# Optimization experiments

Hardware: AMD Instinct MI355X
Metric: run time of the kernel (lower is better)

The kernel has to match this reference:

```python
import jax, jax.numpy as jnp
import numpy as np

D_MODEL = 2048
N_HEADS = 16
D_HEAD = D_MODEL // N_HEADS
D_FF = 4 * D_MODEL
LN_EPS = 1e-5


def setup_inputs() -> dict:
    key = jax.random.key(0)
    ks = jax.random.split(key, 12)
    s = 1.0 / np.sqrt(D_MODEL)
    sf = 1.0 / np.sqrt(D_FF)
    return {
        "x": jax.random.normal(ks[0], (1, 2048, D_MODEL), dtype=jnp.float32),
        "ln1_g": jnp.ones((D_MODEL,), jnp.float32),
        "ln1_b": jnp.zeros((D_MODEL,), jnp.float32),
        # weights stored [in, out] (transpose of torch layout; equivalent under random init)
        "Wq": jax.random.normal(ks[1], (D_MODEL, D_MODEL), jnp.float32) * s,
        "Wk": jax.random.normal(ks[2], (D_MODEL, D_MODEL), jnp.float32) * s,
        "Wv": jax.random.normal(ks[3], (D_MODEL, D_MODEL), jnp.float32) * s,
        "Wp": jax.random.normal(ks[4], (D_MODEL, D_MODEL), jnp.float32) * s,
        "bp": jnp.zeros((D_MODEL,), jnp.float32),
        "ln2_g": jnp.ones((D_MODEL,), jnp.float32),
        "ln2_b": jnp.zeros((D_MODEL,), jnp.float32),
        "W1": jax.random.normal(ks[5], (D_MODEL, D_FF), jnp.float32) * s,
        "b1": jnp.zeros((D_FF,), jnp.float32),
        "W2": jax.random.normal(ks[6], (D_FF, D_MODEL), jnp.float32) * sf,
        "b2": jnp.zeros((D_MODEL,), jnp.float32),
    }


def _layer_norm(x, g, b):
    mu = jnp.mean(x, axis=-1, keepdims=True)
    var = jnp.mean(jnp.square(x - mu), axis=-1, keepdims=True)
    return (x - mu) * jax.lax.rsqrt(var + LN_EPS) * g + b


def _attention(h, Wq, Wk, Wv, Wp, bp):
    B, S, E = h.shape
    q = (h @ Wq).reshape(B, S, N_HEADS, D_HEAD)
    k = (h @ Wk).reshape(B, S, N_HEADS, D_HEAD)
    v = (h @ Wv).reshape(B, S, N_HEADS, D_HEAD)
    # [B, H, S, S] causal scores (matches the naive materialized original)
    scores = jnp.einsum("bqhd,bkhd->bhqk", q, k) / np.sqrt(D_HEAD).astype(np.float32)
    causal = jnp.arange(S)[:, None] >= jnp.arange(S)[None, :]
    scores = jnp.where(causal, scores, -jnp.inf)
    attn = jax.nn.softmax(scores, axis=-1)
    out = jnp.einsum("bhqk,bkhd->bqhd", attn, v).reshape(B, S, E)
    return out @ Wp + bp


def reference(x, ln1_g, ln1_b, Wq, Wk, Wv, Wp, bp, ln2_g, ln2_b, W1, b1, W2, b2):
    # attention branch: x += MHA(LN1(x)); dropout=0 (inference)
    x1 = x + _attention(_layer_norm(x, ln1_g, ln1_b), Wq, Wk, Wv, Wp, bp)
    # ff branch: FeedForward adds its own residual on the normalized input
    g = _layer_norm(x1, ln2_g, ln2_b)
    mlp = jax.nn.gelu(g @ W1 + b1, approximate=False) @ W2 + b2
    return x1 + (g + mlp)
```

## Files before the change

kernel.cpp:

```cpp
#include <hip/hip_runtime.h>
#include <math.h>

typedef unsigned int u32;
typedef unsigned short u16;
typedef __attribute__((ext_vector_type(8))) short short8;
typedef __attribute__((ext_vector_type(4))) float f32x4;

__device__ __forceinline__ u16 f2bf(float f) {
  u32 u = __builtin_bit_cast(u32, f);
  u += 0x7FFFu + ((u >> 16) & 1u);
  return (u16)(u >> 16);
}
__device__ __forceinline__ float bf2f(u16 h) {
  u32 u = ((u32)h) << 16;
  return __builtin_bit_cast(float, u);
}
__device__ __forceinline__ void gload_lds16(const void* g, void* l) {
  __builtin_amdgcn_global_load_lds((const __attribute__((address_space(1))) u32*)g,
                                   (__attribute__((address_space(3))) u32*)l, 16, 0, 0);
}
__device__ __forceinline__ f32x4 mfma16(short8 a, short8 b, f32x4 c) {
  return __builtin_amdgcn_mfma_f32_16x16x32_bf16(a, b, c, 0, 0, 0);
}

__global__ __launch_bounds__(256) void transpose_cast(const float* __restrict__ src,
                                                      u16* __restrict__ dst, int K, int N) {
  __shared__ __attribute__((aligned(16))) u16 tile[64][72];
  const int n0 = blockIdx.x * 64, k0 = blockIdx.y * 64;
  const int t = threadIdx.x;
  const int tr = t >> 4;
  const int tc4 = (t & 15) * 4;
#pragma unroll
  for (int p = 0; p < 4; ++p) {
    int row = p * 16 + tr;
    const float4 v = *(const float4*)(src + (size_t)(k0 + row) * N + n0 + tc4);
    tile[tc4 + 0][row] = f2bf(v.x);
    tile[tc4 + 1][row] = f2bf(v.y);
    tile[tc4 + 2][row] = f2bf(v.z);
    tile[tc4 + 3][row] = f2bf(v.w);
  }
  __syncthreads();
  const int nr = t >> 2;
  const int kc = (t & 3) * 16;
  u16* d = dst + (size_t)(n0 + nr) * K + k0 + kc;
  *(short8*)(d) = *(const short8*)&tile[nr][kc];
  *(short8*)(d + 8) = *(const short8*)&tile[nr][kc + 8];
}

__global__ __launch_bounds__(256) void transpose_v(const u16* __restrict__ qkv,
                                                   u16* __restrict__ vT) {
  __shared__ __attribute__((aligned(16))) u16 tile[64][72];
  const int kv0 = blockIdx.x * 64, d0 = blockIdx.y * 64, h = blockIdx.z;
  const int t = threadIdx.x;
  const int tr = t >> 3;
  const int tc8 = (t & 7) * 8;
#pragma unroll
  for (int p = 0; p < 2; ++p) {
    int row = p * 32 + tr;
    short8 v = *(const short8*)(qkv + (size_t)(kv0 + row) * 6144 + 4096 + h * 128 + d0 + tc8);
#pragma unroll
    for (int j = 0; j < 8; ++j) tile[tc8 + j][row] = (u16)v[j];
  }
  __syncthreads();
  const int dr = t >> 2;
  const int kc = (t & 3) * 16;
  u16* dst = vT + ((size_t)h * 128 + d0 + dr) * 2048 + kv0 + kc;
  *(short8*)dst = *(const short8*)&tile[dr][kc];
  *(short8*)(dst + 8) = *(const short8*)&tile[dr][kc + 8];
}

__global__ __launch_bounds__(256) void ln_kernel(const float* __restrict__ x,
                                                 const float* __restrict__ gw,
                                                 const float* __restrict__ bw,
                                                 u16* __restrict__ out) {
  const int row = blockIdx.x, t = threadIdx.x;
  const float* xr = x + (size_t)row * 2048;
  const float4 v0 = *(const float4*)(xr + t * 8);
  const float4 v1 = *(const float4*)(xr + t * 8 + 4);
  float s = v0.x + v0.y + v0.z + v0.w + v1.x + v1.y + v1.z + v1.w;
  float q = v0.x * v0.x + v0.y * v0.y + v0.z * v0.z + v0.w * v0.w +
            v1.x * v1.x + v1.y * v1.y + v1.z * v1.z + v1.w * v1.w;
#pragma unroll
  for (int w = 32; w; w >>= 1) { s += __shfl_xor(s, w); q += __shfl_xor(q, w); }
  __shared__ float rs[4], rq[4];
  const int wid = t >> 6, lane = t & 63;
  if (!lane) { rs[wid] = s; rq[wid] = q; }
  __syncthreads();
  s = rs[0] + rs[1] + rs[2] + rs[3];
  q = rq[0] + rq[1] + rq[2] + rq[3];
  const float mu = s * (1.f / 2048.f);
  const float var = q * (1.f / 2048.f) - mu * mu;
  const float rstd = rsqrtf(var + 1e-5f);
  const float4 g0 = *(const float4*)(gw + t * 8);
  const float4 g1 = *(const float4*)(gw + t * 8 + 4);
  const float4 b0 = *(const float4*)(bw + t * 8);
  const float4 b1 = *(const float4*)(bw + t * 8 + 4);
  short8 o;
  o[0] = (short)f2bf((v0.x - mu) * rstd * g0.x + b0.x);
  o[1] = (short)f2bf((v0.y - mu) * rstd * g0.y + b0.y);
  o[2] = (short)f2bf((v0.z - mu) * rstd * g0.z + b0.z);
  o[3] = (short)f2bf((v0.w - mu) * rstd * g0.w + b0.w);
  o[4] = (short)f2bf((v1.x - mu) * rstd * g1.x + b1.x);
  o[5] = (short)f2bf((v1.y - mu) * rstd * g1.y + b1.y);
  o[6] = (short)f2bf((v1.z - mu) * rstd * g1.z + b1.z);
  o[7] = (short)f2bf((v1.w - mu) * rstd * g1.w + b1.w);
  *(short8*)(out + (size_t)row * 2048 + t * 8) = o;
}

template <int EPI>
__global__ __launch_bounds__(256) void gemm_kernel(const u16* __restrict__ A,
                                                   const u16* __restrict__ Bt,
                                                   int M, int N, int K, int Kc,
                                                   float* __restrict__ outF,
                                                   u16* __restrict__ outB,
                                                   const float* __restrict__ bias,
                                                   const float* __restrict__ res1,
                                                   const u16* __restrict__ res2,
                                                   float* __restrict__ pA,
                                                   float* __restrict__ pB) {
  __shared__ __attribute__((aligned(16))) u16 lsA[128 * 64];
  __shared__ __attribute__((aligned(16))) u16 lsB[128 * 64];
  const int m0 = blockIdx.y * 128, n0 = blockIdx.x * 128;
  const int tid = threadIdx.x, wid = tid >> 6, lane = tid & 63;
  const int wm = (wid >> 1) * 64, wn = (wid & 1) * 64;
  const int lq = lane & 15, lk = lane >> 4;
  const int rIn = lane >> 3, sIn = lane & 7;
  const int kStart = blockIdx.z * Kc;
  f32x4 acc[4][4] = {};

  for (int kt = kStart; kt < kStart + Kc; kt += 64) {
    if (kt != kStart) __syncthreads();
#pragma unroll
    for (int i = 0; i < 4; ++i) {
      int c = wid * 4 + i;
      int row = c * 8 + rIn;
      int scol = (sIn ^ (row & 7)) * 8;
      gload_lds16(A + (size_t)(m0 + row) * K + kt + scol, lsA + c * 512);
      gload_lds16(Bt + (size_t)(n0 + row) * K + kt + scol, lsB + c * 512);
    }
    __syncthreads();
#pragma unroll
    for (int kk = 0; kk < 2; ++kk) {
      short8 af[4], bfr[4];
#pragma unroll
      for (int i = 0; i < 4; ++i) {
        int ra = wm + i * 16 + lq;
        af[i] = *(const short8*)((const char*)lsA + ra * 128 +
                                 ((kk * 64 + lk * 16) ^ ((ra & 7) << 4)));
        int rb = wn + i * 16 + lq;
        bfr[i] = *(const short8*)((const char*)lsB + rb * 128 +
                                  ((kk * 64 + lk * 16) ^ ((rb & 7) << 4)));
      }
#pragma unroll
      for (int mi = 0; mi < 4; ++mi)
#pragma unroll
        for (int ni = 0; ni < 4; ++ni)
          acc[mi][ni] = mfma16(af[mi], bfr[ni], acc[mi][ni]);
    }
  }
  float* pp = nullptr;
  if (EPI == 4) {
    pp = (blockIdx.z < 2) ? pA : pB;
    pp += (size_t)(blockIdx.z & 1) * ((size_t)M * N);
  }
#pragma unroll
  for (int mi = 0; mi < 4; ++mi) {
#pragma unroll
    for (int ni = 0; ni < 4; ++ni) {
      const int col = n0 + wn + ni * 16 + lq;
#pragma unroll
      for (int r = 0; r < 4; ++r) {
        const int row = m0 + wm + mi * 16 + lk * 4 + r;
        const size_t idx = (size_t)row * N + col;
        float v = acc[mi][ni][r];
        if (EPI == 0) {
          outB[idx] = f2bf(v);
        } else if (EPI == 1) {
          outF[idx] = v + bias[col] + res1[idx];
        } else if (EPI == 2) {
          float xg = v + bias[col];
          outB[idx] = f2bf(0.5f * xg * (1.f + erff(xg * 0.70710678118654752f)));
        } else if (EPI == 3) {
          outF[idx] = v + bias[col] + res1[idx] + bf2f(res2[idx]);
        } else {
          pp[idx] = v;
        }
      }
    }
  }
}

template <int NS, int RES2>
__global__ __launch_bounds__(256) void reduce_kernel(const float* __restrict__ pA,
                                                     const float* __restrict__ pB,
                                                     const float* __restrict__ bias,
                                                     const float* __restrict__ res1,
                                                     const u16* __restrict__ res2,
                                                     float* __restrict__ out,
                                                     int MN, int N) {
  const int i = (blockIdx.x * 256 + threadIdx.x) * 4;
  if (i >= MN) return;
  float4 s = *(const float4*)(pA + i);
  {
    const float4 t = *(const float4*)(pA + MN + i);
    s.x += t.x; s.y += t.y; s.z += t.z; s.w += t.w;
  }
  if (NS == 4) {
    const float4 t0 = *(const float4*)(pB + i);
    const float4 t1 = *(const float4*)(pB + MN + i);
    s.x += t0.x + t1.x; s.y += t0.y + t1.y; s.z += t0.z + t1.z; s.w += t0.w + t1.w;
  }
  const int col = i & (N - 1);
  const float4 bv = *(const float4*)(bias + col);
  const float4 r1 = *(const float4*)(res1 + i);
  float4 o;
  o.x = s.x + bv.x + r1.x;
  o.y = s.y + bv.y + r1.y;
  o.z = s.z + bv.z + r1.z;
  o.w = s.w + bv.w + r1.w;
  if (RES2) {
    const u16* r2 = res2 + i;
    o.x += bf2f(r2[0]); o.y += bf2f(r2[1]); o.z += bf2f(r2[2]); o.w += bf2f(r2[3]);
  }
  *(float4*)(out + i) = o;
}

__global__ __launch_bounds__(256) void attn_kernel(const u16* __restrict__ qkv,
                                                   const u16* __restrict__ vT,
                                                   u16* __restrict__ attnout) {
  __shared__ __attribute__((aligned(16))) u16 lsK[64 * 128];
  __shared__ __attribute__((aligned(16))) u16 lsV[128 * 64];
  __shared__ __attribute__((aligned(16))) u16 lsP[4][16 * 64];
  const int h = blockIdx.y;
  const int qb = blockIdx.x * 64;
  const int tid = threadIdx.x, wid = tid >> 6, lane = tid & 63;
  const int lq = lane & 15, lk = lane >> 4;
  const int qw = qb + wid * 16;

  short8 qf[4];
  {
    const u16* qp = qkv + (size_t)(qw + lq) * 6144 + h * 128;
#pragma unroll
    for (int ks = 0; ks < 4; ++ks) qf[ks] = *(const short8*)(qp + ks * 32 + lk * 8);
  }
  float mreg[4], lreg[4];
  f32x4 o[8];
#pragma unroll
  for (int r = 0; r < 4; ++r) { mreg[r] = -INFINITY; lreg[r] = 0.f; }
#pragma unroll
  for (int dt = 0; dt < 8; ++dt) o[dt] = (f32x4){0.f, 0.f, 0.f, 0.f};

  const int rK = lane >> 4, sK = lane & 15;
  const int rV = lane >> 3, sV = lane & 7;
  const int nkt = qb / 64 + 1;
  for (int kt = 0; kt < nkt; ++kt) {
    const int kv0 = kt * 64;
    if (kt) __syncthreads();
#pragma unroll
    for (int i = 0; i < 4; ++i) {
      int c = wid * 4 + i;
      int rowK = c * 4 + rK;
      gload_lds16(qkv + (size_t)(kv0 + rowK) * 6144 + 2048 + h * 128 + ((sK ^ (rowK & 7)) * 8),
                  lsK + c * 512);
      int rowV = c * 8 + rV;
      gload_lds16(vT + ((size_t)h * 128 + rowV) * 2048 + kv0 + ((sV ^ (rowV & 7)) * 8),
                  lsV + c * 512);
    }
    __syncthreads();

    f32x4 sc[4];
#pragma unroll
    for (int nt = 0; nt < 4; ++nt) sc[nt] = (f32x4){0.f, 0.f, 0.f, 0.f};
#pragma unroll
    for (int ks = 0; ks < 4; ++ks) {
#pragma unroll
      for (int nt = 0; nt < 4; ++nt) {
        int kvr = nt * 16 + lq;
        short8 kf = *(const short8*)((const char*)lsK + kvr * 256 +
                                     ((ks * 64 + lk * 16) ^ ((kvr & 7) << 4)));
        sc[nt] = mfma16(qf[ks], kf, sc[nt]);
      }
    }
    float rmax[4] = {-INFINITY, -INFINITY, -INFINITY, -INFINITY};
#pragma unroll
    for (int nt = 0; nt < 4; ++nt) {
      int kv = kv0 + nt * 16 + lq;
#pragma unroll
      for (int r = 0; r < 4; ++r) {
        int qrow = qw + lk * 4 + r;
        float s = (kv <= qrow) ? sc[nt][r] * 0.08838834764831845f : -INFINITY;
        sc[nt][r] = s;
        rmax[r] = fmaxf(rmax[r], s);
      }
    }
#pragma unroll
    for (int r = 0; r < 4; ++r)
#pragma unroll
      for (int w = 1; w < 16; w <<= 1) rmax[r] = fmaxf(rmax[r], __shfl_xor(rmax[r], w));
    float alpha[4], rsum[4];
#pragma unroll
    for (int r = 0; r < 4; ++r) {
      float mn = fmaxf(mreg[r], rmax[r]);
      alpha[r] = __expf(mreg[r] - mn);
      mreg[r] = mn;
      rsum[r] = 0.f;
    }
    u16* P = &lsP[wid][0];
#pragma unroll
    for (int nt = 0; nt < 4; ++nt) {
#pragma unroll
      for (int r = 0; r < 4; ++r) {
        float p = __expf(sc[nt][r] - mreg[r]);
        rsum[r] += p;
        int prow = lk * 4 + r, pcol = nt * 16 + lq;
        *(u16*)((char*)P + prow * 128 + ((pcol * 2) ^ ((prow & 7) << 4))) = f2bf(p);
      }
    }
#pragma unroll
    for (int r = 0; r < 4; ++r) {
#pragma unroll
      for (int w = 1; w < 16; w <<= 1) rsum[r] += __shfl_xor(rsum[r], w);
      lreg[r] = lreg[r] * alpha[r] + rsum[r];
    }
#pragma unroll
    for (int dt = 0; dt < 8; ++dt)
#pragma unroll
      for (int r = 0; r < 4; ++r) o[dt][r] *= alpha[r];
#pragma unroll
    for (int kk = 0; kk < 2; ++kk) {
      short8 pa = *(const short8*)((const char*)P + lq * 128 +
                                   ((kk * 64 + lk * 16) ^ ((lq & 7) << 4)));
#pragma unroll
      for (int dt = 0; dt < 8; ++dt) {
        int dr = dt * 16 + lq;
        short8 vf = *(const short8*)((const char*)lsV + dr * 128 +
                                     ((kk * 64 + lk * 16) ^ ((dr & 7) << 4)));
        o[dt] = mfma16(pa, vf, o[dt]);
      }
    }
  }
#pragma unroll
  for (int r = 0; r < 4; ++r) {
    float inv = 1.f / lreg[r];
    int row = qw + lk * 4 + r;
    u16* op = attnout + (size_t)row * 2048 + h * 128 + lq;
#pragma unroll
    for (int dt = 0; dt < 8; ++dt) op[dt * 16] = f2bf(o[dt][r] * inv);
  }
}

extern "C" void kernel_launch(void* const* d_in, const int* in_sizes, int n_in,
                              void* d_out, int out_size, void* d_ws, size_t ws_size,
                              hipStream_t stream) {
  (void)in_sizes; (void)n_in; (void)out_size; (void)ws_size;
  const float* x    = (const float*)d_in[0];
  const float* ln1g = (const float*)d_in[1];
  const float* ln1b = (const float*)d_in[2];
  const float* Wq   = (const float*)d_in[3];
  const float* Wk   = (const float*)d_in[4];
  const float* Wv   = (const float*)d_in[5];
  const float* Wp   = (const float*)d_in[6];
  const float* bp   = (const float*)d_in[7];
  const float* ln2g = (const float*)d_in[8];
  const float* ln2b = (const float*)d_in[9];
  const float* W1   = (const float*)d_in[10];
  const float* b1   = (const float*)d_in[11];
  const float* W2   = (const float*)d_in[12];
  const float* b2   = (const float*)d_in[13];
  float* out = (float*)d_out;
  char* ws = (char*)d_ws;

  u16* wqkvT = (u16*)(ws + 0);
  u16* hbuf  = (u16*)(ws + 25165824);
  u16* wpT   = (u16*)(ws + 33554432);
  u16* w1T   = (u16*)(ws + 41943040);
  u16* w2T   = (u16*)(ws + 75497472);
  u16* qkv   = (u16*)(ws + 109051904);
  u16* vT    = (u16*)(ws + 134217728);
  u16* attn  = (u16*)(ws + 142606336);
  float* x1  = (float*)(ws + 150994944);
  u16* g     = (u16*)(ws + 167772160);
  u16* ff1   = (u16*)(ws + 0);
  float* projP = (float*)(ws + 109051904);
  float* ffPA = (float*)(ws + 33554432);
  float* ffPB = (float*)(ws + 109051904);

  dim3 b256(256);
  transpose_cast<<<dim3(32, 32), b256, 0, stream>>>(Wq, wqkvT, 2048, 2048);
  transpose_cast<<<dim3(32, 32), b256, 0, stream>>>(Wk, wqkvT + 2048 * 2048, 2048, 2048);
  transpose_cast<<<dim3(32, 32), b256, 0, stream>>>(Wv, wqkvT + 4096 * 2048, 2048, 2048);
  transpose_cast<<<dim3(32, 32), b256, 0, stream>>>(Wp, wpT, 2048, 2048);
  transpose_cast<<<dim3(128, 32), b256, 0, stream>>>(W1, w1T, 2048, 8192);
  transpose_cast<<<dim3(32, 128), b256, 0, stream>>>(W2, w2T, 8192, 2048);
  ln_kernel<<<2048, b256, 0, stream>>>(x, ln1g, ln1b, hbuf);
  gemm_kernel<0><<<dim3(48, 16), b256, 0, stream>>>(hbuf, wqkvT, 2048, 6144, 2048, 2048,
                                                    nullptr, qkv, nullptr, nullptr, nullptr,
                                                    nullptr, nullptr);
  transpose_v<<<dim3(32, 2, 16), b256, 0, stream>>>(qkv, vT);
  attn_kernel<<<dim3(32, 16), b256, 0, stream>>>(qkv, vT, attn);
  gemm_kernel<4><<<dim3(16, 16, 2), b256, 0, stream>>>(attn, wpT, 2048, 2048, 2048, 1024,
                                                       nullptr, nullptr, nullptr, nullptr,
                                                       nullptr, projP, nullptr);
  reduce_kernel<2, 0><<<4096, b256, 0, stream>>>(projP, nullptr, bp, x, nullptr, x1,
                                                 4194304, 2048);
  ln_kernel<<<2048, b256, 0, stream>>>(x1, ln2g, ln2b, g);
  gemm_kernel<2><<<dim3(64, 16), b256, 0, stream>>>(g, w1T, 2048, 8192, 2048, 2048,
                                                    nullptr, ff1, b1, nullptr, nullptr,
                                                    nullptr, nullptr);
  gemm_kernel<4><<<dim3(16, 16, 4), b256, 0, stream>>>(ff1, w2T, 2048, 2048, 8192, 2048,
                                                       nullptr, nullptr, nullptr, nullptr,
                                                       nullptr, ffPA, ffPB);
  reduce_kernel<4, 1><<<4096, b256, 0, stream>>>(ffPA, ffPB, b2, x1, g, out,
                                                 4194304, 2048);
}
```

Baseline: 456.3 us.

## Replace GEMM with 256x128-tile, 512-thread triple-buffered pipelined kernel

Replaces the single-buffered 128x128 GEMM with a 512-thread kernel that computes 256x128 tiles. It keeps three LDS stages, issues global-to-LDS loads two k-tiles ahead, and interleaves them with the MFMA phases using barriers, vmcnt waits and setprio. The W2 GEMM split-K drops from 4 to 2 slices, so the reduce kernel now reads only two partial buffers. The larger LDS footprint (about 144KB) may limit occupancy, and the fewer, larger blocks could underfill the CUs on the smaller GEMMs.

```diff
diff --git a/kernel.cpp b/kernel.cpp
--- a/kernel.cpp
+++ b/kernel.cpp
@@ -108,80 +108,110 @@
 }
 
 template <int EPI>
-__global__ __launch_bounds__(256) void gemm_kernel(const u16* __restrict__ A,
-                                                   const u16* __restrict__ Bt,
-                                                   int M, int N, int K, int Kc,
-                                                   float* __restrict__ outF,
-                                                   u16* __restrict__ outB,
-                                                   const float* __restrict__ bias,
-                                                   const float* __restrict__ res1,
-                                                   const u16* __restrict__ res2,
-                                                   float* __restrict__ pA,
-                                                   float* __restrict__ pB) {
-  __shared__ __attribute__((aligned(16))) u16 lsA[128 * 64];
-  __shared__ __attribute__((aligned(16))) u16 lsB[128 * 64];
-  const int m0 = blockIdx.y * 128, n0 = blockIdx.x * 128;
+__global__ __launch_bounds__(512, 2) void gemm2(const u16* __restrict__ A,
+                                                const u16* __restrict__ Bt,
+                                                int M, int N, int K, int Kc,
+                                                u16* __restrict__ outB,
+                                                const float* __restrict__ bias,
+                                                float* __restrict__ pA) {
+  __shared__ __attribute__((aligned(16))) u16 lds[3 * 24576];
+  const int m0 = blockIdx.y * 256, n0 = blockIdx.x * 128;
   const int tid = threadIdx.x, wid = tid >> 6, lane = tid & 63;
-  const int wm = (wid >> 1) * 64, wn = (wid & 1) * 64;
+  const int wr = wid >> 1, wc = wid & 1;
   const int lq = lane & 15, lk = lane >> 4;
-  const int rIn = lane >> 3, sIn = lane & 7;
   const int kStart = blockIdx.z * Kc;
+  const int NT = Kc / 64;
+
+  size_t aoff[4], boff[2];
+#pragma unroll
+  for (int s = 0; s < 4; ++s) {
+    int c = s * 512 + tid;
+    int row = c >> 3, col = ((c & 7) ^ (row & 7)) * 8;
+    aoff[s] = (size_t)(m0 + row) * K + col;
+  }
+#pragma unroll
+  for (int s = 0; s < 2; ++s) {
+    int c = s * 512 + tid;
+    int row = c >> 3, col = ((c & 7) ^ (row & 7)) * 8;
+    boff[s] = (size_t)(n0 + row) * K + col;
+  }
+  const int dstc = wid * 512 + lane * 8;
+
+#define STAGE_A(s, t2) \
+  gload_lds16(A + aoff[s] + (size_t)(kStart + (t2) * 64), \
+              lds + ((t2) % 3) * 24576 + (s) * 4096 + dstc)
+#define STAGE_B(s, t2) \
+  gload_lds16(Bt + boff[s] + (size_t)(kStart + (t2) * 64), \
+              lds + ((t2) % 3) * 24576 + 16384 + (s) * 4096 + dstc)
+
+  STAGE_A(0, 0); STAGE_A(1, 0); STAGE_A(2, 0); STAGE_A(3, 0); STAGE_B(0, 0); STAGE_B(1, 0);
+  STAGE_A(0, 1); STAGE_A(1, 1); STAGE_A(2, 1); STAGE_A(3, 1); STAGE_B(0, 1); STAGE_B(1, 1);
+  asm volatile("s_waitcnt vmcnt(6)" ::: "memory");
+  __builtin_amdgcn_s_barrier();
+  __builtin_amdgcn_sched_barrier(0);
+
   f32x4 acc[4][4] = {};
-
-  for (int kt = kStart; kt < kStart + Kc; kt += 64) {
-    if (kt != kStart) __syncthreads();
-#pragma unroll
-    for (int i = 0; i < 4; ++i) {
-      int c = wid * 4 + i;
-      int row = c * 8 + rIn;
-      int scol = (sIn ^ (row & 7)) * 8;
-      gload_lds16(A + (size_t)(m0 + row) * K + kt + scol, lsA + c * 512);
-      gload_lds16(Bt + (size_t)(n0 + row) * K + kt + scol, lsB + c * 512);
-    }
-    __syncthreads();
-#pragma unroll
-    for (int kk = 0; kk < 2; ++kk) {
-      short8 af[4], bfr[4];
-#pragma unroll
-      for (int i = 0; i < 4; ++i) {
-        int ra = wm + i * 16 + lq;
-        af[i] = *(const short8*)((const char*)lsA + ra * 128 +
-                                 ((kk * 64 + lk * 16) ^ ((ra & 7) << 4)));
-        int rb = wn + i * 16 + lq;
-        bfr[i] = *(const short8*)((const char*)lsB + rb * 128 +
-                                  ((kk * 64 + lk * 16) ^ ((rb & 7) << 4)));
-      }
+  int cur = 0;
+  for (int t = 0; t < NT; ++t) {
+    const char* bufA = (const char*)lds + cur * 49152;
+    const char* bufB = bufA + 32768;
+    const int t2 = t + 2;
+    const bool st = t2 < NT;
+    const int xorq = (lq & 7) << 4;
+#pragma unroll
+    for (int ph = 0; ph < 2; ++ph) {
+      short8 af[4], bf[4];
+#pragma unroll
+      for (int mi = 0; mi < 4; ++mi) {
+        int ar = wr * 64 + mi * 16 + lq;
+        af[mi] = *(const short8*)(bufA + ar * 128 + ((ph * 64 + lk * 16) ^ xorq));
+      }
+#pragma unroll
+      for (int ni = 0; ni < 4; ++ni) {
+        int br = wc * 64 + ni * 16 + lq;
+        bf[ni] = *(const short8*)(bufB + br * 128 + ((ph * 64 + lk * 16) ^ xorq));
+      }
+      if (st) {
+        if (ph == 0) { STAGE_A(0, t2); STAGE_A(1, t2); STAGE_A(2, t2); }
+        else         { STAGE_A(3, t2); STAGE_B(0, t2); STAGE_B(1, t2); }
+      }
+      __builtin_amdgcn_s_barrier();
+      __builtin_amdgcn_s_setprio(1);
 #pragma unroll
       for (int mi = 0; mi < 4; ++mi)
 #pragma unroll
         for (int ni = 0; ni < 4; ++ni)
-          acc[mi][ni] = mfma16(af[mi], bfr[ni], acc[mi][ni]);
-    }
-  }
+          acc[mi][ni] = mfma16(af[mi], bf[ni], acc[mi][ni]);
+      __builtin_amdgcn_s_setprio(0);
+      if (ph == 1) {
+        if (st) asm volatile("s_waitcnt vmcnt(6)" ::: "memory");
+        else    asm volatile("s_waitcnt vmcnt(0)" ::: "memory");
+      }
+      __builtin_amdgcn_s_barrier();
+      __builtin_amdgcn_sched_barrier(0);
+    }
+    cur = (cur == 2) ? 0 : cur + 1;
+  }
+#undef STAGE_A
+#undef STAGE_B
+
   float* pp = nullptr;
-  if (EPI == 4) {
-    pp = (blockIdx.z < 2) ? pA : pB;
-    pp += (size_t)(blockIdx.z & 1) * ((size_t)M * N);
-  }
+  if (EPI == 4) pp = pA + (size_t)blockIdx.z * ((size_t)M * N);
 #pragma unroll
   for (int mi = 0; mi < 4; ++mi) {
 #pragma unroll
     for (int ni = 0; ni < 4; ++ni) {
-      const int col = n0 + wn + ni * 16 + lq;
+      const int col = n0 + wc * 64 + ni * 16 + lq;
 #pragma unroll
       for (int r = 0; r < 4; ++r) {
-        const int row = m0 + wm + mi * 16 + lk * 4 + r;
+        const int row = m0 + wr * 64 + mi * 16 + lk * 4 + r;
         const size_t idx = (size_t)row * N + col;
         float v = acc[mi][ni][r];
         if (EPI == 0) {
           outB[idx] = f2bf(v);
-        } else if (EPI == 1) {
-          outF[idx] = v + bias[col] + res1[idx];
         } else if (EPI == 2) {
           float xg = v + bias[col];
           outB[idx] = f2bf(0.5f * xg * (1.f + erff(xg * 0.70710678118654752f)));
-        } else if (EPI == 3) {
-          outF[idx] = v + bias[col] + res1[idx] + bf2f(res2[idx]);
         } else {
           pp[idx] = v;
         }
@@ -190,9 +220,8 @@
   }
 }
 
-template <int NS, int RES2>
+template <int RES2>
 __global__ __launch_bounds__(256) void reduce_kernel(const float* __restrict__ pA,
-                                                     const float* __restrict__ pB,
                                                      const float* __restrict__ bias,
                                                      const float* __restrict__ res1,
                                                      const u16* __restrict__ res2,
@@ -204,11 +233,6 @@
   {
     const float4 t = *(const float4*)(pA + MN + i);
     s.x += t.x; s.y += t.y; s.z += t.z; s.w += t.w;
-  }
-  if (NS == 4) {
-    const float4 t0 = *(const float4*)(pB + i);
-    const float4 t1 = *(const float4*)(pB + MN + i);
-    s.x += t0.x + t1.x; s.y += t0.y + t1.y; s.z += t0.z + t1.z; s.w += t0.w + t1.w;
   }
   const int col = i & (N - 1);
   const float4 bv = *(const float4*)(bias + col);
@@ -382,10 +406,9 @@
   u16* g     = (u16*)(ws + 167772160);
   u16* ff1   = (u16*)(ws + 0);
   float* projP = (float*)(ws + 109051904);
-  float* ffPA = (float*)(ws + 33554432);
-  float* ffPB = (float*)(ws + 109051904);
-
-  dim3 b256(256);
+  float* ffP = (float*)(ws + 33554432);
+
+  dim3 b256(256), b512(512);
   transpose_cast<<<dim3(32, 32), b256, 0, stream>>>(Wq, wqkvT, 2048, 2048);
   transpose_cast<<<dim3(32, 32), b256, 0, stream>>>(Wk, wqkvT + 2048 * 2048, 2048, 2048);
   transpose_cast<<<dim3(32, 32), b256, 0, stream>>>(Wv, wqkvT + 4096 * 2048, 2048, 2048);
@@ -393,23 +416,17 @@
   transpose_cast<<<dim3(128, 32), b256, 0, stream>>>(W1, w1T, 2048, 8192);
   transpose_cast<<<dim3(32, 128), b256, 0, stream>>>(W2, w2T, 8192, 2048);
   ln_kernel<<<2048, b256, 0, stream>>>(x, ln1g, ln1b, hbuf);
-  gemm_kernel<0><<<dim3(48, 16), b256, 0, stream>>>(hbuf, wqkvT, 2048, 6144, 2048, 2048,
-                                                    nullptr, qkv, nullptr, nullptr, nullptr,
-                                                    nullptr, nullptr);
+  gemm2<0><<<dim3(48, 8, 1), b512, 0, stream>>>(hbuf, wqkvT, 2048, 6144, 2048, 2048,
+                                                qkv, nullptr, nullptr);
   transpose_v<<<dim3(32, 2, 16), b256, 0, stream>>>(qkv, vT);
   attn_kernel<<<dim3(32, 16), b256, 0, stream>>>(qkv, vT, attn);
-  gemm_kernel<4><<<dim3(16, 16, 2), b256, 0, stream>>>(attn, wpT, 2048, 2048, 2048, 1024,
-                                                       nullptr, nullptr, nullptr, nullptr,
-                                                       nullptr, projP, nullptr);
-  reduce_kernel<2, 0><<<4096, b256, 0, stream>>>(projP, nullptr, bp, x, nullptr, x1,
-                                                 4194304, 2048);
+  gemm2<4><<<dim3(16, 8, 2), b512, 0, stream>>>(attn, wpT, 2048, 2048, 2048, 1024,
+                                                nullptr, nullptr, projP);
+  reduce_kernel<0><<<4096, b256, 0, stream>>>(projP, bp, x, nullptr, x1, 4194304, 2048);
   ln_kernel<<<2048, b256, 0, stream>>>(x1, ln2g, ln2b, g);
-  gemm_kernel<2><<<dim3(64, 16), b256, 0, stream>>>(g, w1T, 2048, 8192, 2048, 2048,
-                                                    nullptr, ff1, b1, nullptr, nullptr,
-                                                    nullptr, nullptr);
-  gemm_kernel<4><<<dim3(16, 16, 4), b256, 0, stream>>>(ff1, w2T, 2048, 2048, 8192, 2048,
-                                                       nullptr, nullptr, nullptr, nullptr,
-                                                       nullptr, ffPA, ffPB);
-  reduce_kernel<4, 1><<<4096, b256, 0, stream>>>(ffPA, ffPB, b2, x1, g, out,
-                                                 4194304, 2048);
-}
+  gemm2<2><<<dim3(64, 8, 1), b512, 0, stream>>>(g, w1T, 2048, 8192, 2048, 2048,
+                                                ff1, b1, nullptr);
+  gemm2<4><<<dim3(16, 8, 2), b512, 0, stream>>>(ff1, w2T, 2048, 2048, 8192, 4096,
+                                                nullptr, nullptr, ffP);
+  reduce_kernel<1><<<4096, b256, 0, stream>>>(ffP, b2, x1, g, out, 4194304, 2048);
+}
```

Measured after the change: 444.6 us. 2.6% less time.
